# Performance work log

Hardware: AMD Instinct MI355X
Metric: run time of the kernel (lower is better)

The kernel has to match this reference:

```python
import jax, jax.numpy as jnp
import numpy as np

N_NODES = 100000
N_EDGES = 1600000
N_DATE = 5000  # last N_DATE nodes are date nodes [0,0,1]
D_IN = 128
D_H = 128
N_CLASSES = 16
MLP_HID = 8


def setup_inputs() -> dict:
    key = jax.random.key(0)
    ks = jax.random.split(key, 12)
    feature = jax.random.normal(ks[0], (N_NODES, D_IN), dtype=jnp.float32)
    edge_weight = jax.random.uniform(ks[1], (N_EDGES,), dtype=jnp.float32)
    src = jax.random.randint(ks[2], (N_EDGES,), 0, N_NODES, dtype=jnp.int32)
    dst = jax.random.randint(ks[3], (N_EDGES,), 0, N_NODES, dtype=jnp.int32)
    # node_type one-hot: regular nodes [1,0,0], last N_DATE nodes are date nodes [0,0,1]
    nt = np.zeros((N_NODES, 3), dtype=np.int32)
    nt[: N_NODES - N_DATE, 0] = 1
    nt[N_NODES - N_DATE :, 2] = 1
    node_type = jnp.asarray(nt)
    # GraphConv weights (xavier uniform) + zero bias, DGL convention: h @ W, W:[in,out]
    def xavier(k, fan_in, fan_out):
        lim = float(np.sqrt(6.0 / (fan_in + fan_out)))
        return jax.random.uniform(k, (fan_in, fan_out), jnp.float32, -lim, lim)
    W0 = xavier(ks[4], D_IN, D_H)
    b0 = jnp.zeros((D_H,), jnp.float32)
    W1 = xavier(ks[5], D_H, D_H)
    b1 = jnp.zeros((D_H,), jnp.float32)
    mlp_w1 = xavier(ks[6], D_H, MLP_HID)
    mlp_b1 = jnp.zeros((MLP_HID,), jnp.float32)
    mlp_w2 = xavier(ks[7], MLP_HID, N_CLASSES)
    mlp_b2 = jnp.zeros((N_CLASSES,), jnp.float32)
    return {
        "feature": feature, "edge_weight": edge_weight, "src": src, "dst": dst,
        "node_type": node_type, "W0": W0, "b0": b0, "W1": W1, "b1": b1,
        "mlp_w1": mlp_w1, "mlp_b1": mlp_b1, "mlp_w2": mlp_w2, "mlp_b2": mlp_b2,
    }


def reference(feature, edge_weight, src, dst, node_type,
              W0, b0, W1, b1, mlp_w1, mlp_b1, mlp_w2, mlp_b2):
    n = feature.shape[0]
    ones_e = jnp.ones_like(edge_weight)
    # unweighted degrees (DGL norm='both'), clamped to >= 1
    deg_out = jnp.clip(jax.ops.segment_sum(ones_e, src, num_segments=n), 1.0)
    deg_in = jnp.clip(jax.ops.segment_sum(ones_e, dst, num_segments=n), 1.0)
    norm_src = deg_out ** -0.5  # [N]
    norm_dst = deg_in ** -0.5   # [N]

    def graph_conv(h, W, b):
        hn = h * norm_src[:, None]                      # D_out^{-1/2} src scaling
        msg = hn[src] * edge_weight[:, None]            # [E, d] edge-weighted gather
        agg = jax.ops.segment_sum(msg, dst, num_segments=n)  # scatter-add
        return (agg * norm_dst[:, None]) @ W + b        # D_in^{-1/2}, then linear

    h = jax.nn.relu(graph_conv(feature, W0, b0))
    h = jax.nn.relu(graph_conv(h, W1, b1))

    # sum-pool over date nodes ([0,0,1]) == tail slice in original layout
    date_mask = ((node_type[:, 0] == 0) & (node_type[:, 1] == 0) & (node_type[:, 2] == 1)).astype(h.dtype)
    cnt = date_mask.sum()
    pooled = (h * date_mask[:, None]).sum(axis=0) / cnt  # [d_h]

    hid = jax.nn.relu(pooled @ mlp_w1 + mlp_b1)
    return hid @ mlp_w2 + mlp_b2  # [num_classes]
```

## Files before the change

### kernel.cpp

```cpp
#include <hip/hip_runtime.h>
#include <hip/hip_fp16.h>
#include <hip/hip_fp8.h>
#include <stdint.h>

#define D 128
#define GT 16
#define SLOTS 48
#define EPB 4096
#define PTB 1024
#define CAPE 5120
#define MAXB 400
#define MAXDATE 8192
#define WPN 16384

typedef _Float16 f16x8 __attribute__((ext_vector_type(8)));
typedef float    f32x4 __attribute__((ext_vector_type(4)));

__device__ __forceinline__ float fp8_dec(unsigned char b) {
    __hip_fp8_e4m3 t;
    t.__x = b;
    return (float)t;
}

__global__ __launch_bounds__(PTB) void partition_kernel(
    const int* __restrict__ src, const int* __restrict__ dst, const float* __restrict__ ew,
    int* __restrict__ cursorA, int* __restrict__ cursorB,
    int2* __restrict__ ebuf, int* __restrict__ sbuf, int E, int nbk) {
    __shared__ int histA[MAXB], histB[MAXB], baseA[MAXB], baseB[MAXB];
    int tid = threadIdx.x;
    for (int i = tid; i < nbk; i += PTB) { histA[i] = 0; histB[i] = 0; }
    __syncthreads();
    int e0 = blockIdx.x * EPB;
    int dcache[EPB / PTB], scache[EPB / PTB];
    float wcache[EPB / PTB];
    #pragma unroll
    for (int i = 0; i < EPB / PTB; ++i) {
        int e = e0 + i * PTB + tid;
        bool ok = e < E;
        dcache[i] = ok ? dst[e] : -1;
        scache[i] = ok ? src[e] : 0;
        wcache[i] = ok ? ew[e] : 0.f;
        if (ok) {
            atomicAdd(&histA[dcache[i] >> 8], 1);
            atomicAdd(&histB[scache[i] >> 8], 1);
        }
    }
    __syncthreads();
    for (int i = tid; i < nbk; i += PTB) {
        baseA[i] = atomicAdd(&cursorA[i], histA[i]);
        baseB[i] = atomicAdd(&cursorB[i], histB[i]);
        histA[i] = 0; histB[i] = 0;
    }
    __syncthreads();
    #pragma unroll
    for (int i = 0; i < EPB / PTB; ++i) {
        if (dcache[i] >= 0) {
            int d = dcache[i], s = scache[i];
            int bA = d >> 8;
            int pA = baseA[bA] + atomicAdd(&histA[bA], 1);
            if (pA < CAPE) ebuf[(size_t)bA * CAPE + pA] =
                make_int2(s | ((d & 255) << 17), __float_as_int(wcache[i]));
            int bB = s >> 8;
            int pB = baseB[bB] + atomicAdd(&histB[bB], 1);
            if (pB < CAPE) sbuf[(size_t)bB * CAPE + pB] = s;
        }
    }
}

__global__ __launch_bounds__(256) void build_count_kernel(
    const int2* __restrict__ ebuf, const int* __restrict__ cursorA,
    const int* __restrict__ sbuf, const int* __restrict__ cursorB,
    int2* __restrict__ ell, int* __restrict__ deg_in, int* __restrict__ deg_out,
    int n, int nbk) {
    __shared__ int lcur[256];
    int tid = threadIdx.x;
    lcur[tid] = 0;
    __syncthreads();
    if (blockIdx.x < (unsigned)nbk) {
        int b = blockIdx.x;
        int cntE = min(cursorA[b], CAPE);
        const int2* buf = ebuf + (size_t)b * CAPE;
        for (int i = tid; i < cntE; i += 256) {
            int2 r = buf[i];
            int s = r.x & 0x1FFFF;
            int dlow = (r.x >> 17) & 255;
            int slot = atomicAdd(&lcur[dlow], 1);
            int node = (b << 8) + dlow;
            if (slot < SLOTS) ell[(size_t)node * SLOTS + slot] = make_int2(s, r.y);
        }
        __syncthreads();
        int v = (b << 8) + tid;
        if (v < n) deg_in[v] = lcur[tid];
    } else {
        int b = blockIdx.x - nbk;
        int cntS = min(cursorB[b], CAPE);
        const int* buf = sbuf + (size_t)b * CAPE;
        for (int i = tid; i < cntS; i += 256) {
            atomicAdd(&lcur[buf[i] & 255], 1);
        }
        __syncthreads();
        int v = (b << 8) + tid;
        if (v < n) deg_out[v] = lcur[tid];
    }
}

__global__ void norm_flag_kernel(const int* __restrict__ deg_out, const int* __restrict__ deg_in,
                                 const int* __restrict__ node_type,
                                 float* __restrict__ norm_src, float* __restrict__ norm_dst,
                                 int* __restrict__ list, int* __restrict__ cnt, int n) {
    int v = blockIdx.x * blockDim.x + threadIdx.x;
    if (v < n) {
        float d_o = (float)max(deg_out[v], 1);
        float d_i = (float)max(deg_in[v], 1);
        norm_src[v] = 1.0f / sqrtf(d_o);
        norm_dst[v] = 1.0f / sqrtf(d_i);
        int t0 = node_type[v * 3 + 0];
        int t1 = node_type[v * 3 + 1];
        int t2 = node_type[v * 3 + 2];
        if (t0 == 0 && t1 == 0 && t2 == 1) {
            int idx = atomicAdd(cnt, 1);
            list[idx] = v;
        }
    }
}

__global__ __launch_bounds__(256) void wpack_kernel(const float* __restrict__ W,
                                                    _Float16* __restrict__ wp,
                                                    int* __restrict__ cursorAB,
                                                    float* __restrict__ pooled,
                                                    int* __restrict__ cnt) {
    int tid = threadIdx.x;
    if (blockIdx.x == 0) {
        for (int i = tid; i < 2 * MAXB; i += 256) cursorAB[i] = 0;
        if (tid < D) pooled[tid] = 0.f;
        if (tid == 0) *cnt = 0;
    }
    int base = blockIdx.x * 256 + tid;
    for (int idx = base; idx < WPN; idx += gridDim.x * 256) {
        int j = idx & 7;
        int l = (idx >> 3) & 63;
        int c = (idx >> 9) & 7;
        int k0b = idx >> 12;
        int q = l >> 4, r = l & 15;
        float w = W[(k0b * 32 + q * 8 + j) * 128 + c * 16 + r];
        _Float16 hi = (_Float16)w;
        wp[idx] = hi;
        wp[idx + WPN] = (_Float16)(w - (float)hi);
    }
}

__global__ __launch_bounds__(256) void gemm_mfma_kernel(
    const float* __restrict__ X, const float* __restrict__ ns,
    const _Float16* __restrict__ wp, unsigned char* __restrict__ P8, int n) {
    int lane = threadIdx.x & 63;
    int wib  = threadIdx.x >> 6;
    int q = lane >> 4, r = lane & 15;
    int row0 = blockIdx.x * 128 + wib * 32;
    if (row0 >= n) return;
    int ra = min(row0 + r,      n - 1);
    int rb = min(row0 + 16 + r, n - 1);
    float sa = ns[ra];
    float sb = ns[rb];

    f32x4 acc[2][8];
    #pragma unroll
    for (int t = 0; t < 2; ++t)
        #pragma unroll
        for (int c = 0; c < 8; ++c)
            acc[t][c] = (f32x4){0.f, 0.f, 0.f, 0.f};

    for (int k0 = 0; k0 < 128; k0 += 32) {
        float4 xa0 = *(const float4*)&X[(size_t)ra * 128 + k0 + q * 8];
        float4 xa1 = *(const float4*)&X[(size_t)ra * 128 + k0 + q * 8 + 4];
        float4 xb0 = *(const float4*)&X[(size_t)rb * 128 + k0 + q * 8];
        float4 xb1 = *(const float4*)&X[(size_t)rb * 128 + k0 + q * 8 + 4];
        f16x8 a0, a1;
        a0[0] = (_Float16)(xa0.x * sa); a0[1] = (_Float16)(xa0.y * sa);
        a0[2] = (_Float16)(xa0.z * sa); a0[3] = (_Float16)(xa0.w * sa);
        a0[4] = (_Float16)(xa1.x * sa); a0[5] = (_Float16)(xa1.y * sa);
        a0[6] = (_Float16)(xa1.z * sa); a0[7] = (_Float16)(xa1.w * sa);
        a1[0] = (_Float16)(xb0.x * sb); a1[1] = (_Float16)(xb0.y * sb);
        a1[2] = (_Float16)(xb0.z * sb); a1[3] = (_Float16)(xb0.w * sb);
        a1[4] = (_Float16)(xb1.x * sb); a1[5] = (_Float16)(xb1.y * sb);
        a1[6] = (_Float16)(xb1.z * sb); a1[7] = (_Float16)(xb1.w * sb);
        const _Float16* wb = wp + (size_t)(k0 >> 5) * 4096 + lane * 8;
        #pragma unroll
        for (int c = 0; c < 8; ++c) {
            f16x8 bh = *(const f16x8*)&wb[c * 512];
            f16x8 bl = *(const f16x8*)&wb[c * 512 + WPN];
            acc[0][c] = __builtin_amdgcn_mfma_f32_16x16x32_f16(a0, bh, acc[0][c], 0, 0, 0);
            acc[0][c] = __builtin_amdgcn_mfma_f32_16x16x32_f16(a0, bl, acc[0][c], 0, 0, 0);
            acc[1][c] = __builtin_amdgcn_mfma_f32_16x16x32_f16(a1, bh, acc[1][c], 0, 0, 0);
            acc[1][c] = __builtin_amdgcn_mfma_f32_16x16x32_f16(a1, bl, acc[1][c], 0, 0, 0);
        }
    }

    #pragma unroll
    for (int t = 0; t < 2; ++t) {
        #pragma unroll
        for (int j = 0; j < 4; ++j) {
            int row = row0 + t * 16 + q * 4 + j;
            if (row < n) {
                #pragma unroll
                for (int c = 0; c < 8; ++c) {
                    __hip_fp8_e4m3 qv((float)acc[t][c][j]);
                    P8[(size_t)row * 128 + c * 16 + r] = qv.__x;
                }
            }
        }
    }
}

__global__ __launch_bounds__(256) void gather1_kernel(
    const unsigned char* __restrict__ P8, const int* __restrict__ deg_in,
    const int2* __restrict__ ell, const float* __restrict__ norm_src,
    const float* __restrict__ norm_dst, const float* __restrict__ bias,
    __half* __restrict__ h1, int n) {
    int wave = (blockIdx.x * 256 + threadIdx.x) >> 6;
    int lane = threadIdx.x & 63;
    if (wave >= n) return;
    int v = __builtin_amdgcn_readfirstlane(wave);
    int m = min(deg_in[v], SLOTS);
    const int2* row = ell + (size_t)v * SLOTS;
    int half = lane >> 5;
    int l32  = lane & 31;
    const unsigned int* P32 = (const unsigned int*)P8;
    float4 acc = make_float4(0.f, 0.f, 0.f, 0.f);
    for (int e = 0; e < m; e += 4) {
        int4 qa = *(const int4*)&row[e];
        int4 qb = *(const int4*)&row[e + 2];
        int2 p0 = half ? make_int2(qa.z, qa.w) : make_int2(qa.x, qa.y);
        int2 p1 = half ? make_int2(qb.z, qb.w) : make_int2(qb.x, qb.y);
        bool v0 = (e + half) < m;
        bool v1 = (e + 2 + half) < m;
        int s0 = v0 ? p0.x : 0;
        int s1 = v1 ? p1.x : 0;
        unsigned int r0 = P32[(size_t)s0 * 32 + l32];
        unsigned int r1 = P32[(size_t)s1 * 32 + l32];
        float w0 = v0 ? __int_as_float(p0.y) * __builtin_amdgcn_readfirstlane(0x3f800000 ? 1.f : 1.f) : 0.f;
        w0 = v0 ? __int_as_float(p0.y) : 0.f;
        float w1 = v1 ? __int_as_float(p1.y) : 0.f;
        acc.x = fmaf(w0, fp8_dec(r0 & 0xff),         acc.x);
        acc.y = fmaf(w0, fp8_dec((r0 >> 8) & 0xff),  acc.y);
        acc.z = fmaf(w0, fp8_dec((r0 >> 16) & 0xff), acc.z);
        acc.w = fmaf(w0, fp8_dec(r0 >> 24),          acc.w);
        acc.x = fmaf(w1, fp8_dec(r1 & 0xff),         acc.x);
        acc.y = fmaf(w1, fp8_dec((r1 >> 8) & 0xff),  acc.y);
        acc.z = fmaf(w1, fp8_dec((r1 >> 16) & 0xff), acc.z);
        acc.w = fmaf(w1, fp8_dec(r1 >> 24),          acc.w);
    }
    acc.x += __shfl_xor(acc.x, 32);
    acc.y += __shfl_xor(acc.y, 32);
    acc.z += __shfl_xor(acc.z, 32);
    acc.w += __shfl_xor(acc.w, 32);
    if (half == 0) {
        float nd = norm_dst[v];
        float ns = norm_src[v];
        float4 b4 = ((const float4*)bias)[l32];
        float ra = fmaxf(fmaf(acc.x, nd, b4.x), 0.f) * ns;
        float rb = fmaxf(fmaf(acc.y, nd, b4.y), 0.f) * ns;
        float rc = fmaxf(fmaf(acc.z, nd, b4.z), 0.f) * ns;
        float rd = fmaxf(fmaf(acc.w, nd, b4.w), 0.f) * ns;
        __half2 h0 = __floats2half2_rn(ra, rb);
        __half2 h1v = __floats2half2_rn(rc, rd);
        uint2 u;
        u.x = *(unsigned int*)&h0;
        u.y = *(unsigned int*)&h1v;
        ((uint2*)h1)[(size_t)v * 32 + l32] = u;
    }
}

__global__ __launch_bounds__(256) void gather2_list_kernel(
    const __half* __restrict__ h, const int* __restrict__ deg_in,
    const int2* __restrict__ ell, const float* __restrict__ norm_dst,
    const int* __restrict__ list, const int* __restrict__ cnt,
    float* __restrict__ out) {
    int wave = (blockIdx.x * 256 + threadIdx.x) >> 6;
    int lane = threadIdx.x & 63;
    if (wave >= min(*cnt, MAXDATE)) return;
    int v = __builtin_amdgcn_readfirstlane(list[wave]);
    int m = min(deg_in[v], SLOTS);
    const int2* row = ell + (size_t)v * SLOTS;
    int half = lane >> 5;
    int l32  = lane & 31;
    float4 acc = make_float4(0.f, 0.f, 0.f, 0.f);
    for (int e = 0; e < m; e += 4) {
        int4 qa = *(const int4*)&row[e];
        int4 qb = *(const int4*)&row[e + 2];
        int2 p0 = half ? make_int2(qa.z, qa.w) : make_int2(qa.x, qa.y);
        int2 p1 = half ? make_int2(qb.z, qb.w) : make_int2(qb.x, qb.y);
        bool v0 = (e + half) < m;
        bool v1 = (e + 2 + half) < m;
        int s0 = v0 ? p0.x : 0;
        int s1 = v1 ? p1.x : 0;
        float2 raw0 = ((const float2*)h)[(size_t)s0 * 32 + l32];
        float2 raw1 = ((const float2*)h)[(size_t)s1 * 32 + l32];
        float w0 = v0 ? __int_as_float(p0.y) : 0.f;
        float w1 = v1 ? __int_as_float(p1.y) : 0.f;
        float2 a01 = __half22float2(*(const __half2*)&raw0.x);
        float2 a23 = __half22float2(*(const __half2*)&raw0.y);
        float2 b01 = __half22float2(*(const __half2*)&raw1.x);
        float2 b23 = __half22float2(*(const __half2*)&raw1.y);
        acc.x = fmaf(w0, a01.x, acc.x); acc.x = fmaf(w1, b01.x, acc.x);
        acc.y = fmaf(w0, a01.y, acc.y); acc.y = fmaf(w1, b01.y, acc.y);
        acc.z = fmaf(w0, a23.x, acc.z); acc.z = fmaf(w1, b23.x, acc.z);
        acc.w = fmaf(w0, a23.y, acc.w); acc.w = fmaf(w1, b23.y, acc.w);
    }
    acc.x += __shfl_xor(acc.x, 32);
    acc.y += __shfl_xor(acc.y, 32);
    acc.z += __shfl_xor(acc.z, 32);
    acc.w += __shfl_xor(acc.w, 32);
    if (half == 0) {
        float nd = norm_dst[v];
        ((float4*)(out + (size_t)wave * D))[l32] =
            make_float4(acc.x * nd, acc.y * nd, acc.z * nd, acc.w * nd);
    }
}

__global__ __launch_bounds__(256) void gemm_pool_kernel(
    const float* __restrict__ X, const float* __restrict__ W,
    const float* __restrict__ bias, const int* __restrict__ cnt,
    float* __restrict__ pooled) {
    __shared__ float rows[4][GT * D];
    int lane = threadIdx.x & 63;
    int wib  = threadIdx.x >> 6;
    int tile = blockIdx.x * 4 + wib;
    int t0 = tile * GT;
    int m = min(*cnt, MAXDATE);
    if (t0 >= m) return;

    float* rw = rows[wib];
    const float2* X2 = (const float2*)X;
    #pragma unroll
    for (int t = 0; t < GT; ++t) {
        int i = t0 + t;
        float2 r = (i < m) ? X2[(size_t)i * 64 + lane] : make_float2(0.f, 0.f);
        *(float2*)&rw[t * D + 2 * lane] = r;
    }
    __builtin_amdgcn_wave_barrier();

    float2 bb = ((const float2*)bias)[lane];
    float2 acc[GT];
    #pragma unroll
    for (int t = 0; t < GT; ++t) acc[t] = make_float2(0.f, 0.f);

    const float2* W2 = (const float2*)W;
    for (int k = 0; k < D; k += 4) {
        float2 w0 = W2[(k + 0) * 64 + lane];
        float2 w1 = W2[(k + 1) * 64 + lane];
        float2 w2 = W2[(k + 2) * 64 + lane];
        float2 w3 = W2[(k + 3) * 64 + lane];
        #pragma unroll
        for (int t = 0; t < GT; ++t) {
            float4 r = *(const float4*)&rw[t * D + k];
            acc[t].x = fmaf(r.x, w0.x, acc[t].x); acc[t].y = fmaf(r.x, w0.y, acc[t].y);
            acc[t].x = fmaf(r.y, w1.x, acc[t].x); acc[t].y = fmaf(r.y, w1.y, acc[t].y);
            acc[t].x = fmaf(r.z, w2.x, acc[t].x); acc[t].y = fmaf(r.z, w2.y, acc[t].y);
            acc[t].x = fmaf(r.w, w3.x, acc[t].x); acc[t].y = fmaf(r.w, w3.y, acc[t].y);
        }
    }

    float psx = 0.f, psy = 0.f;
    #pragma unroll
    for (int t = 0; t < GT; ++t) {
        if (t0 + t < m) {
            psx += fmaxf(acc[t].x + bb.x, 0.f);
            psy += fmaxf(acc[t].y + bb.y, 0.f);
        }
    }
    atomicAdd(&pooled[2 * lane + 0], psx);
    atomicAdd(&pooled[2 * lane + 1], psy);
}

__global__ void mlp_kernel(const float* __restrict__ pooled, const int* __restrict__ cnt,
                           const float* __restrict__ w1, const float* __restrict__ b1,
                           const float* __restrict__ w2, const float* __restrict__ b2,
                           float* __restrict__ out) {
    __shared__ float hid[8];
    int t = threadIdx.x;
    float inv = 1.0f / (float)(*cnt);
    if (t < 8) {
        float a = b1[t];
        for (int k = 0; k < 128; ++k) a = fmaf(pooled[k] * inv, w1[k * 8 + t], a);
        hid[t] = fmaxf(a, 0.f);
    }
    __syncthreads();
    if (t < 16) {
        float a = b2[t];
        for (int j = 0; j < 8; ++j) a = fmaf(hid[j], w2[j * 16 + t], a);
        out[t] = a;
    }
}

extern "C" void kernel_launch(void* const* d_in, const int* in_sizes, int n_in,
                              void* d_out, int out_size, void* d_ws, size_t ws_size,
                              hipStream_t stream) {
    const float* feature   = (const float*)d_in[0];
    const float* ew        = (const float*)d_in[1];
    const int*   src       = (const int*)d_in[2];
    const int*   dst       = (const int*)d_in[3];
    const int*   node_type = (const int*)d_in[4];
    const float* W0        = (const float*)d_in[5];
    const float* b0        = (const float*)d_in[6];
    const float* W1        = (const float*)d_in[7];
    const float* b1        = (const float*)d_in[8];
    const float* mw1       = (const float*)d_in[9];
    const float* mb1       = (const float*)d_in[10];
    const float* mw2       = (const float*)d_in[11];
    const float* mb2       = (const float*)d_in[12];
    float* out = (float*)d_out;

    const int n = in_sizes[0] / D;
    const int E = in_sizes[1];
    const int NBK = (n + 255) >> 8;

    char* ws = (char*)d_ws;
    size_t off = 0;
    auto alloc = [&](size_t bytes) -> void* {
        void* p = ws + off;
        off = (off + bytes + 255) & ~(size_t)255;
        return p;
    };
    int*           cursorAB = (int*)alloc(2 * MAXB * 4);
    int*           deg_in   = (int*)alloc((size_t)n * 4);
    int*           deg_out  = (int*)alloc((size_t)n * 4);
    float*         norm_src = (float*)alloc((size_t)n * 4);
    float*         norm_dst = (float*)alloc((size_t)n * 4);
    int*           list     = (int*)alloc((size_t)n * 4);
    int2*          ell      = (int2*)alloc(((size_t)n * SLOTS + 8) * 8);
    int2*          ebuf     = (int2*)alloc((size_t)NBK * CAPE * 8);
    int*           sbuf     = (int*)alloc((size_t)NBK * CAPE * 4);
    unsigned char* P8       = (unsigned char*)alloc((size_t)n * D);
    __half*        h1       = (__half*)alloc((size_t)n * D * 2);
    _Float16*      wp       = (_Float16*)alloc(2 * WPN * 2);
    float*         pooled   = (float*)alloc(D * 4);
    int*           cnt      = (int*)alloc(256);
    float*         agg      = (float*)sbuf;

    int* cursorA = cursorAB;
    int* cursorB = cursorAB + MAXB;

    const int TB = 256;
    int pblk = (E + EPB - 1) / EPB;
    int nblk = (n + TB - 1) / TB;

    wpack_kernel<<<16, TB, 0, stream>>>(W0, wp, cursorAB, pooled, cnt);
    partition_kernel<<<pblk, PTB, 0, stream>>>(src, dst, ew, cursorA, cursorB, ebuf, sbuf, E, NBK);
    build_count_kernel<<<2 * NBK, TB, 0, stream>>>(ebuf, cursorA, sbuf, cursorB,
                                                   ell, deg_in, deg_out, n, NBK);
    norm_flag_kernel<<<nblk, TB, 0, stream>>>(deg_out, deg_in, node_type,
                                              norm_src, norm_dst, list, cnt, n);

    gemm_mfma_kernel<<<(n + 127) / 128, TB, 0, stream>>>(feature, norm_src, wp, P8, n);

    gather1_kernel<<<(n * 64 + TB - 1) / TB, TB, 0, stream>>>(
        P8, deg_in, ell, norm_src, norm_dst, b0, h1, n);

    gather2_list_kernel<<<(MAXDATE * 64) / TB, TB, 0, stream>>>(
        h1, deg_in, ell, norm_dst, list, cnt, agg);
    gemm_pool_kernel<<<((MAXDATE + GT - 1) / GT + 3) / 4, TB, 0, stream>>>(agg, W1, b1, cnt, pooled);

    mlp_kernel<<<1, 64, 0, stream>>>(pooled, cnt, mw1, mb1, mw2, mb2, out);
}
```

Before: 313.7 us.

## Compute layer-1 output only for in-neighbours of date nodes

Adds a mark kernel that flags every source node that feeds a date node, and gather1 now returns early for unflagged nodes. Only those rows of h1 are ever read by the layer-2 gather, so most of the layer-1 gather work is skipped. The fp8 decode also moves to the packed cvt_pk_f32_fp8 builtin. The cost is an extra kernel launch, a per-node flag write, and a dependence on the ELL truncation at SLOTS matching between the mark and gather2 kernels.

```diff
diff --git a/kernel.cpp b/kernel.cpp
--- a/kernel.cpp
+++ b/kernel.cpp
@@ -15,12 +15,7 @@
 
 typedef _Float16 f16x8 __attribute__((ext_vector_type(8)));
 typedef float    f32x4 __attribute__((ext_vector_type(4)));
-
-__device__ __forceinline__ float fp8_dec(unsigned char b) {
-    __hip_fp8_e4m3 t;
-    t.__x = b;
-    return (float)t;
-}
+typedef float    f32x2 __attribute__((ext_vector_type(2)));
 
 __global__ __launch_bounds__(PTB) void partition_kernel(
     const int* __restrict__ src, const int* __restrict__ dst, const float* __restrict__ ew,
@@ -107,13 +102,15 @@
 __global__ void norm_flag_kernel(const int* __restrict__ deg_out, const int* __restrict__ deg_in,
                                  const int* __restrict__ node_type,
                                  float* __restrict__ norm_src, float* __restrict__ norm_dst,
-                                 int* __restrict__ list, int* __restrict__ cnt, int n) {
+                                 int* __restrict__ list, int* __restrict__ cnt,
+                                 unsigned char* __restrict__ flag, int n) {
     int v = blockIdx.x * blockDim.x + threadIdx.x;
     if (v < n) {
         float d_o = (float)max(deg_out[v], 1);
         float d_i = (float)max(deg_in[v], 1);
         norm_src[v] = 1.0f / sqrtf(d_o);
         norm_dst[v] = 1.0f / sqrtf(d_i);
+        flag[v] = 0;
         int t0 = node_type[v * 3 + 0];
         int t1 = node_type[v * 3 + 1];
         int t2 = node_type[v * 3 + 2];
@@ -121,6 +118,21 @@
             int idx = atomicAdd(cnt, 1);
             list[idx] = v;
         }
+    }
+}
+
+__global__ __launch_bounds__(256) void mark_kernel(
+    const int* __restrict__ list, const int* __restrict__ cnt,
+    const int2* __restrict__ ell, const int* __restrict__ deg_in,
+    unsigned char* __restrict__ flag) {
+    int wave = (blockIdx.x * 256 + threadIdx.x) >> 6;
+    int lane = threadIdx.x & 63;
+    if (wave >= min(*cnt, MAXDATE)) return;
+    int v = __builtin_amdgcn_readfirstlane(list[wave]);
+    int m = min(deg_in[v], SLOTS);
+    if (lane < m) {
+        int s = ell[(size_t)v * SLOTS + lane].x;
+        flag[s] = 1;
     }
 }
 
@@ -215,11 +227,12 @@
     const unsigned char* __restrict__ P8, const int* __restrict__ deg_in,
     const int2* __restrict__ ell, const float* __restrict__ norm_src,
     const float* __restrict__ norm_dst, const float* __restrict__ bias,
-    __half* __restrict__ h1, int n) {
+    const unsigned char* __restrict__ flag, __half* __restrict__ h1, int n) {
     int wave = (blockIdx.x * 256 + threadIdx.x) >> 6;
     int lane = threadIdx.x & 63;
     if (wave >= n) return;
     int v = __builtin_amdgcn_readfirstlane(wave);
+    if (flag[v] == 0) return;
     int m = min(deg_in[v], SLOTS);
     const int2* row = ell + (size_t)v * SLOTS;
     int half = lane >> 5;
@@ -237,17 +250,16 @@
         int s1 = v1 ? p1.x : 0;
         unsigned int r0 = P32[(size_t)s0 * 32 + l32];
         unsigned int r1 = P32[(size_t)s1 * 32 + l32];
-        float w0 = v0 ? __int_as_float(p0.y) * __builtin_amdgcn_readfirstlane(0x3f800000 ? 1.f : 1.f) : 0.f;
-        w0 = v0 ? __int_as_float(p0.y) : 0.f;
+        float w0 = v0 ? __int_as_float(p0.y) : 0.f;
         float w1 = v1 ? __int_as_float(p1.y) : 0.f;
-        acc.x = fmaf(w0, fp8_dec(r0 & 0xff),         acc.x);
-        acc.y = fmaf(w0, fp8_dec((r0 >> 8) & 0xff),  acc.y);
-        acc.z = fmaf(w0, fp8_dec((r0 >> 16) & 0xff), acc.z);
-        acc.w = fmaf(w0, fp8_dec(r0 >> 24),          acc.w);
-        acc.x = fmaf(w1, fp8_dec(r1 & 0xff),         acc.x);
-        acc.y = fmaf(w1, fp8_dec((r1 >> 8) & 0xff),  acc.y);
-        acc.z = fmaf(w1, fp8_dec((r1 >> 16) & 0xff), acc.z);
-        acc.w = fmaf(w1, fp8_dec(r1 >> 24),          acc.w);
+        f32x2 c0 = __builtin_amdgcn_cvt_pk_f32_fp8((int)r0, false);
+        f32x2 c1 = __builtin_amdgcn_cvt_pk_f32_fp8((int)r0, true);
+        f32x2 d0 = __builtin_amdgcn_cvt_pk_f32_fp8((int)r1, false);
+        f32x2 d1 = __builtin_amdgcn_cvt_pk_f32_fp8((int)r1, true);
+        acc.x = fmaf(w0, c0[0], acc.x); acc.x = fmaf(w1, d0[0], acc.x);
+        acc.y = fmaf(w0, c0[1], acc.y); acc.y = fmaf(w1, d0[1], acc.y);
+        acc.z = fmaf(w0, c1[0], acc.z); acc.z = fmaf(w1, d1[0], acc.z);
+        acc.w = fmaf(w0, c1[1], acc.w); acc.w = fmaf(w1, d1[1], acc.w);
     }
     acc.x += __shfl_xor(acc.x, 32);
     acc.y += __shfl_xor(acc.y, 32);
@@ -427,6 +439,7 @@
     float*         norm_src = (float*)alloc((size_t)n * 4);
     float*         norm_dst = (float*)alloc((size_t)n * 4);
     int*           list     = (int*)alloc((size_t)n * 4);
+    unsigned char* flag     = (unsigned char*)alloc((size_t)n);
     int2*          ell      = (int2*)alloc(((size_t)n * SLOTS + 8) * 8);
     int2*          ebuf     = (int2*)alloc((size_t)NBK * CAPE * 8);
     int*           sbuf     = (int*)alloc((size_t)NBK * CAPE * 4);
@@ -449,12 +462,13 @@
     build_count_kernel<<<2 * NBK, TB, 0, stream>>>(ebuf, cursorA, sbuf, cursorB,
                                                    ell, deg_in, deg_out, n, NBK);
     norm_flag_kernel<<<nblk, TB, 0, stream>>>(deg_out, deg_in, node_type,
-                                              norm_src, norm_dst, list, cnt, n);
+                                              norm_src, norm_dst, list, cnt, flag, n);
+    mark_kernel<<<(MAXDATE * 64) / TB, TB, 0, stream>>>(list, cnt, ell, deg_in, flag);
 
     gemm_mfma_kernel<<<(n + 127) / 128, TB, 0, stream>>>(feature, norm_src, wp, P8, n);
 
     gather1_kernel<<<(n * 64 + TB - 1) / TB, TB, 0, stream>>>(
-        P8, deg_in, ell, norm_src, norm_dst, b0, h1, n);
+        P8, deg_in, ell, norm_src, norm_dst, b0, flag, h1, n);
 
     gather2_list_kernel<<<(MAXDATE * 64) / TB, TB, 0, stream>>>(
         h1, deg_in, ell, norm_dst, list, cnt, agg);
```

Result: faster. 290.7 us (-7.3%).
